# Kernel optimization log

Hardware: AMD Instinct MI355X
Metric: run time of the kernel (lower is better)

Reference implementation:

```python
import jax, jax.numpy as jnp
import numpy as np

B, NPTS, H, O, L, PDIM, CDIM = 16, 20000, 128, 4, 6, 8, 3
K = 3  # number of learnable sine terms in Rowdy activation


def setup_inputs() -> dict:
    key = jax.random.key(0)
    ks = jax.random.split(key, 12)
    sc = lambda fan: 1.0 / np.sqrt(fan)
    return {
        "coords": jax.random.normal(ks[0], (B, NPTS, CDIM), dtype=jnp.float32),
        "sdf": jax.random.normal(ks[1], (B, NPTS, 1), dtype=jnp.float32),
        "params": jax.random.normal(ks[2], (B, PDIM), dtype=jnp.float32),
        # branch MLP: PDIM -> H (xL hidden) -> H*O
        "branch_W0": jax.random.normal(ks[3], (PDIM, H)) * sc(PDIM),
        "branch_Wr": jax.random.normal(ks[4], (L - 1, H, H)) * sc(H),
        "branch_b": jnp.zeros((L, H)),
        "branch_Wout": jax.random.normal(ks[5], (H, H * O)) * sc(H),
        "branch_bout": jnp.zeros((H * O,)),
        # trunk MLP: (CDIM+1) -> H (xL) with Rowdy activations
        "trunk_W0": jax.random.normal(ks[6], (CDIM + 1, H)) * sc(CDIM + 1),
        "trunk_Wr": jax.random.normal(ks[7], (L - 1, H, H)) * sc(H),
        "trunk_b": jnp.zeros((L, H)),
        "rowdy_a": 0.1 * jax.random.normal(ks[8], (L, K, H)),
        "final_W": jax.random.normal(ks[9], (H, H)) * sc(H),
        "final_b": jnp.zeros((H,)),
    }


def _rowdy(z, a):
    # Rowdy activation: tanh(z) + sum_k a_k * sin(k*z); a: (K, H)
    out = jnp.tanh(z)
    for k in range(a.shape[0]):
        out = out + a[k] * jnp.sin((k + 1.0) * z)
    return out


def reference(coords, sdf, params, branch_W0, branch_Wr, branch_b,
              branch_Wout, branch_bout, trunk_W0, trunk_Wr, trunk_b,
              rowdy_a, final_W, final_b):
    # ---- branch tower (records post-activation hiddens) ----
    h = jnp.tanh(params @ branch_W0 + branch_b[0])        # (B, H)
    hiddens = [h]
    for i in range(1, L):
        h = jnp.tanh(h @ branch_Wr[i - 1] + branch_b[i])
        hiddens.append(h)
    branch_out = h @ branch_Wout + branch_bout             # (B, H*O)
    # cumulative skip sums S_i = sum_{j<=i} hidden_j
    S = [hiddens[0]]
    for i in range(1, L):
        S.append(hiddens[i] + S[-1])
    # ---- trunk tower with fusion by accumulated branch features ----
    x = jnp.concatenate([coords, sdf], axis=-1)            # (B, NPTS, CDIM+1)
    for i in range(L):
        W = trunk_W0 if i == 0 else trunk_Wr[i - 1]
        x = _rowdy(x @ W + trunk_b[i], rowdy_a[i])         # (B, NPTS, H)
        x = x * S[i][:, None, :]                           # broadcast multiply
    YL = x @ final_W + final_b                             # (B, NPTS, H)
    ZL = branch_out.reshape(B, O, H)
    # sum(ZL * YL, -1) as batched contraction over H
    return jnp.einsum('boh,bnh->bno', ZL, YL)              # (B, NPTS, O)
```

## Files before the change

kernel.cpp:

```cpp
#include <hip/hip_runtime.h>
#include <hip/hip_bf16.h>
#include <stdint.h>

#define B_    16
#define NPTS_ 20000
#define H_    128
#define O_    4
#define L_    6
#define PDIM_ 8
#define K_    3

#define TPTS 64
#define KSTR 136
#define TILES_PER_B ((NPTS_ + TPTS - 1) / TPTS)

typedef __attribute__((ext_vector_type(8))) short short8;
typedef __attribute__((ext_vector_type(4))) float f32x4;
typedef __attribute__((ext_vector_type(4))) unsigned short us4;

__device__ __forceinline__ uint16_t f2bf(float x) {
    uint32_t u = __float_as_uint(x);
    uint32_t r = u + 0x7FFFu + ((u >> 16) & 1u);
    return (uint16_t)(r >> 16);
}
__device__ __forceinline__ float bf2f(uint16_t h) {
    return __uint_as_float(((uint32_t)h) << 16);
}

__device__ __forceinline__ float rowdy_act(float z, float a0, float a1, float a2) {
    float e  = __expf(2.f * z);
    float th = 1.f - 2.f * __builtin_amdgcn_rcpf(e + 1.f);
    float s1 = __sinf(z);
    float c1 = __cosf(z);
    float s2 = 2.f * s1 * c1;
    float s3 = s1 * (3.f - 4.f * s1 * s1);
    return th + a0 * s1 + a1 * s2 + a2 * s3;
}
__device__ __forceinline__ void act_split(float z, float a0, float a1, float a2,
                                          float s, uint16_t& h, uint16_t& l) {
    float x = rowdy_act(z, a0, a1, a2) * s;
    h = f2bf(x);
    l = f2bf(x - bf2f(h));
}

__global__ void prep_w(const float* __restrict__ tWr,
                       uint16_t* __restrict__ WtHi, uint16_t* __restrict__ WtLo) {
    const int bid = blockIdx.x;
    const int l   = bid >> 7;
    const int j   = bid & 127;
    const int k   = threadIdx.x;
    float w = tWr[((size_t)l * H_ + k) * H_ + j];
    uint16_t h = f2bf(w);
    uint16_t lo = f2bf(w - bf2f(h));
    WtHi[((size_t)l * H_ + j) * H_ + k] = h;
    WtLo[((size_t)l * H_ + j) * H_ + k] = lo;
}

__global__ void branch_kernel(
    const float* __restrict__ params,
    const float* __restrict__ bW0, const float* __restrict__ bWr,
    const float* __restrict__ bb,  const float* __restrict__ bWout,
    const float* __restrict__ bbout,
    const float* __restrict__ fW,  const float* __restrict__ fb,
    float* __restrict__ S, float* __restrict__ M, float* __restrict__ c0)
{
    const int b = blockIdx.x;
    const int j = threadIdx.x;
    __shared__ float h[H_];
    __shared__ float zl[O_][H_];

    float z = bb[j];
    #pragma unroll
    for (int k = 0; k < PDIM_; ++k)
        z = fmaf(params[b * PDIM_ + k], bW0[k * H_ + j], z);
    float hv = tanhf(z);
    float srun = hv;
    h[j] = hv;
    S[(0 * B_ + b) * H_ + j] = srun;

    for (int i = 1; i < L_; ++i) {
        __syncthreads();
        const float* W = bWr + (size_t)(i - 1) * H_ * H_;
        float zz = bb[i * H_ + j];
        for (int k = 0; k < H_; ++k)
            zz = fmaf(h[k], W[k * H_ + j], zz);
        __syncthreads();
        hv = tanhf(zz);
        h[j] = hv;
        srun += hv;
        S[(i * B_ + b) * H_ + j] = srun;
    }
    __syncthreads();

    #pragma unroll
    for (int o = 0; o < O_; ++o) {
        float acc = bbout[o * H_ + j];
        for (int k = 0; k < H_; ++k)
            acc = fmaf(h[k], bWout[(size_t)k * (H_ * O_) + o * H_ + j], acc);
        zl[o][j] = acc;
    }
    __syncthreads();

    float m[O_] = {0.f, 0.f, 0.f, 0.f};
    for (int hh = 0; hh < H_; ++hh) {
        float w = fW[j * H_ + hh];
        #pragma unroll
        for (int o = 0; o < O_; ++o)
            m[o] = fmaf(w, zl[o][hh], m[o]);
    }
    #pragma unroll
    for (int o = 0; o < O_; ++o)
        M[((size_t)b * H_ + j) * O_ + o] = m[o];

    if (j < O_) {
        float acc = 0.f;
        for (int hh = 0; hh < H_; ++hh)
            acc = fmaf(fb[hh], zl[j][hh], acc);
        c0[b * O_ + j] = acc;
    }
}

__global__ __launch_bounds__(256, 4) void trunk_mfma(
    const float* __restrict__ coords, const float* __restrict__ sdf,
    const float* __restrict__ tW0,    const float* __restrict__ tb,
    const float* __restrict__ ra,     const float* __restrict__ S,
    const float* __restrict__ M,      const float* __restrict__ c0,
    const uint16_t* __restrict__ WtHi, const uint16_t* __restrict__ WtLo,
    float* __restrict__ out)
{
    __shared__ __align__(16) uint16_t Xhi[TPTS][KSTR];
    __shared__ __align__(16) uint16_t Xlo[TPTS][KSTR];

    const int blk  = blockIdx.x;
    const int b    = blk / TILES_PER_B;
    const int tile = blk % TILES_PER_B;
    const int p0   = tile * TPTS;
    const int t    = threadIdx.x;

    {
        const int p = t >> 2;
        const int q = t & 3;
        int pg = p0 + p;
        int pc = pg < NPTS_ ? pg : NPTS_ - 1;
        size_t gp = (size_t)b * NPTS_ + pc;
        float in0 = coords[gp * 3 + 0], in1 = coords[gp * 3 + 1];
        float in2 = coords[gp * 3 + 2], in3 = sdf[gp];
        #pragma unroll
        for (int jj = 0; jj < 32; jj += 4) {
            const int j = q * 32 + jj;
            float4 w0 = *(const float4*)(tW0 + 0 * H_ + j);
            float4 w1 = *(const float4*)(tW0 + 1 * H_ + j);
            float4 w2 = *(const float4*)(tW0 + 2 * H_ + j);
            float4 w3 = *(const float4*)(tW0 + 3 * H_ + j);
            float4 bv = *(const float4*)(tb + j);
            float4 A0 = *(const float4*)(ra + 0 * H_ + j);
            float4 A1 = *(const float4*)(ra + 1 * H_ + j);
            float4 A2 = *(const float4*)(ra + 2 * H_ + j);
            float4 Sv = *(const float4*)(S + b * H_ + j);
            float z0 = fmaf(in3, w3.x, fmaf(in2, w2.x, fmaf(in1, w1.x, fmaf(in0, w0.x, bv.x))));
            float z1 = fmaf(in3, w3.y, fmaf(in2, w2.y, fmaf(in1, w1.y, fmaf(in0, w0.y, bv.y))));
            float z2 = fmaf(in3, w3.z, fmaf(in2, w2.z, fmaf(in1, w1.z, fmaf(in0, w0.z, bv.z))));
            float z3 = fmaf(in3, w3.w, fmaf(in2, w2.w, fmaf(in1, w1.w, fmaf(in0, w0.w, bv.w))));
            us4 h4, l4;
            uint16_t hh, ll;
            act_split(z0, A0.x, A1.x, A2.x, Sv.x, hh, ll); h4[0] = hh; l4[0] = ll;
            act_split(z1, A0.y, A1.y, A2.y, Sv.y, hh, ll); h4[1] = hh; l4[1] = ll;
            act_split(z2, A0.z, A1.z, A2.z, Sv.z, hh, ll); h4[2] = hh; l4[2] = ll;
            act_split(z3, A0.w, A1.w, A2.w, Sv.w, hh, ll); h4[3] = hh; l4[3] = ll;
            *(us4*)(&Xhi[p][j]) = h4;
            *(us4*)(&Xlo[p][j]) = l4;
        }
    }
    __syncthreads();

    const int ln    = t & 63;
    const int wv    = t >> 6;
    const int l15   = ln & 15;
    const int l4    = ln >> 4;
    const int jbase = wv * 32;

    for (int layer = 1; layer < L_; ++layer) {
        f32x4 acc[2][4];
        #pragma unroll
        for (int jf = 0; jf < 2; ++jf) {
            const int j = jbase + jf * 16 + l4 * 4;
            float4 bv = *(const float4*)(tb + layer * H_ + j);
            #pragma unroll
            for (int pf = 0; pf < 4; ++pf)
                acc[jf][pf] = (f32x4){bv.x, bv.y, bv.z, bv.w};
        }
        const uint16_t* WH = WtHi + (size_t)(layer - 1) * H_ * H_;
        const uint16_t* WL = WtLo + (size_t)(layer - 1) * H_ * H_;
        #pragma unroll
        for (int ks = 0; ks < 4; ++ks) {
            const int kpos = ks * 32 + l4 * 8;
            short8 aH[2], aL[2];
            #pragma unroll
            for (int jf = 0; jf < 2; ++jf) {
                const int j = jbase + jf * 16 + l15;
                aH[jf] = *(const short8*)(WH + (size_t)j * H_ + kpos);
                aL[jf] = *(const short8*)(WL + (size_t)j * H_ + kpos);
            }
            #pragma unroll
            for (int pf = 0; pf < 4; ++pf) {
                const int prow = pf * 16 + l15;
                short8 bH = *(const short8*)(&Xhi[prow][kpos]);
                short8 bL = *(const short8*)(&Xlo[prow][kpos]);
                #pragma unroll
                for (int jf = 0; jf < 2; ++jf) {
                    acc[jf][pf] = __builtin_amdgcn_mfma_f32_16x16x32_bf16(aH[jf], bH, acc[jf][pf], 0, 0, 0);
                    acc[jf][pf] = __builtin_amdgcn_mfma_f32_16x16x32_bf16(aH[jf], bL, acc[jf][pf], 0, 0, 0);
                    acc[jf][pf] = __builtin_amdgcn_mfma_f32_16x16x32_bf16(aL[jf], bH, acc[jf][pf], 0, 0, 0);
                }
            }
        }
        __syncthreads();

        #pragma unroll
        for (int jf = 0; jf < 2; ++jf) {
            const int j = jbase + jf * 16 + l4 * 4;
            float4 A0 = *(const float4*)(ra + (layer * K_ + 0) * H_ + j);
            float4 A1 = *(const float4*)(ra + (layer * K_ + 1) * H_ + j);
            float4 A2 = *(const float4*)(ra + (layer * K_ + 2) * H_ + j);
            float4 Sv = *(const float4*)(S + (layer * B_ + b) * H_ + j);
            #pragma unroll
            for (int pf = 0; pf < 4; ++pf) {
                const int prow = pf * 16 + l15;
                us4 h4, l4v;
                uint16_t hh, ll;
                act_split(acc[jf][pf][0], A0.x, A1.x, A2.x, Sv.x, hh, ll); h4[0] = hh; l4v[0] = ll;
                act_split(acc[jf][pf][1], A0.y, A1.y, A2.y, Sv.y, hh, ll); h4[1] = hh; l4v[1] = ll;
                act_split(acc[jf][pf][2], A0.z, A1.z, A2.z, Sv.z, hh, ll); h4[2] = hh; l4v[2] = ll;
                act_split(acc[jf][pf][3], A0.w, A1.w, A2.w, Sv.w, hh, ll); h4[3] = hh; l4v[3] = ll;
                *(us4*)(&Xhi[prow][j]) = h4;
                *(us4*)(&Xlo[prow][j]) = l4v;
            }
        }
        __syncthreads();
    }

    {
        const int p = t >> 2;
        const int o = t & 3;
        float acc = c0[b * O_ + o];
        const float* Mb = M + (size_t)b * H_ * O_;
        #pragma unroll 4
        for (int k = 0; k < H_; k += 8) {
            short8 h8 = *(const short8*)(&Xhi[p][k]);
            short8 l8 = *(const short8*)(&Xlo[p][k]);
            #pragma unroll
            for (int e = 0; e < 8; ++e) {
                float xv = bf2f((uint16_t)h8[e]) + bf2f((uint16_t)l8[e]);
                acc = fmaf(xv, Mb[(k + e) * O_ + o], acc);
            }
        }
        int gp = p0 + p;
        if (gp < NPTS_)
            out[((size_t)b * NPTS_ + gp) * O_ + o] = acc;
    }
}

extern "C" void kernel_launch(void* const* d_in, const int* in_sizes, int n_in,
                              void* d_out, int out_size, void* d_ws, size_t ws_size,
                              hipStream_t stream) {
    const float* coords  = (const float*)d_in[0];
    const float* sdf     = (const float*)d_in[1];
    const float* params  = (const float*)d_in[2];
    const float* bW0     = (const float*)d_in[3];
    const float* bWr     = (const float*)d_in[4];
    const float* bb      = (const float*)d_in[5];
    const float* bWout   = (const float*)d_in[6];
    const float* bbout   = (const float*)d_in[7];
    const float* tW0     = (const float*)d_in[8];
    const float* tWr     = (const float*)d_in[9];
    const float* tb      = (const float*)d_in[10];
    const float* ra      = (const float*)d_in[11];
    const float* fW      = (const float*)d_in[12];
    const float* fb      = (const float*)d_in[13];
    float* out = (float*)d_out;

    float* S  = (float*)d_ws;
    float* M  = S + (size_t)L_ * B_ * H_;
    float* c0 = M + (size_t)B_ * H_ * O_;
    uint16_t* WtHi = (uint16_t*)(c0 + B_ * O_);
    uint16_t* WtLo = WtHi + (size_t)(L_ - 1) * H_ * H_;

    prep_w<<<dim3((L_ - 1) * H_), dim3(H_), 0, stream>>>(tWr, WtHi, WtLo);
    branch_kernel<<<dim3(B_), dim3(H_), 0, stream>>>(
        params, bW0, bWr, bb, bWout, bbout, fW, fb, S, M, c0);
    trunk_mfma<<<dim3(B_ * TILES_PER_B), dim3(256), 0, stream>>>(
        coords, sdf, tW0, tb, ra, S, M, c0, WtHi, WtLo, out);
}
```

Baseline: 522.4 us.

## Store weights and activations in MFMA fragment order and pack bf16 via hardware cvt

Lays out the hi/lo bf16 weight copies in global memory and the activation tile in shared memory in MFMA fragment order. Each lane now does contiguous 16-byte loads with no padded strides. Activation packing uses v_cvt_pk_bf16_f32 instead of manual rounding. The hi weight fragments for all k-steps are also preloaded into registers before the MFMA loop. This is meant to cut LDS bank conflicts, address arithmetic and conversion ALU work, at the cost of more register pressure and a more complex index mapping.

```diff
diff --git a/kernel.cpp b/kernel.cpp
--- a/kernel.cpp
+++ b/kernel.cpp
@@ -11,20 +11,27 @@
 #define K_    3
 
 #define TPTS 64
-#define KSTR 136
 #define TILES_PER_B ((NPTS_ + TPTS - 1) / TPTS)
 
 typedef __attribute__((ext_vector_type(8))) short short8;
 typedef __attribute__((ext_vector_type(4))) float f32x4;
-typedef __attribute__((ext_vector_type(4))) unsigned short us4;
-
+typedef __attribute__((ext_vector_type(2))) uint32_t u32x2;
+typedef __attribute__((ext_vector_type(4))) uint32_t u32x4;
+
+#define FRAG(ks, pf, pl, lane) ((((((ks)*4 + (pf))*2 + (pl))*64) + (lane))*8)
+
+__device__ __forceinline__ uint32_t cvt_pk_bf16(float a, float b) {
+    uint32_t d;
+    asm("v_cvt_pk_bf16_f32 %0, %1, %2" : "=v"(d) : "v"(a), "v"(b));
+    return d;
+}
+__device__ __forceinline__ float bf2f(uint16_t h) {
+    return __uint_as_float(((uint32_t)h) << 16);
+}
 __device__ __forceinline__ uint16_t f2bf(float x) {
     uint32_t u = __float_as_uint(x);
     uint32_t r = u + 0x7FFFu + ((u >> 16) & 1u);
     return (uint16_t)(r >> 16);
-}
-__device__ __forceinline__ float bf2f(uint16_t h) {
-    return __uint_as_float(((uint32_t)h) << 16);
 }
 
 __device__ __forceinline__ float rowdy_act(float z, float a0, float a1, float a2) {
@@ -36,24 +43,47 @@
     float s3 = s1 * (3.f - 4.f * s1 * s1);
     return th + a0 * s1 + a1 * s2 + a2 * s3;
 }
-__device__ __forceinline__ void act_split(float z, float a0, float a1, float a2,
-                                          float s, uint16_t& h, uint16_t& l) {
-    float x = rowdy_act(z, a0, a1, a2) * s;
-    h = f2bf(x);
-    l = f2bf(x - bf2f(h));
+
+__device__ __forceinline__ void act_pack4(const f32x4& v,
+                                          const float4& A0, const float4& A1,
+                                          const float4& A2, const float4& Sv,
+                                          u32x2& hi, u32x2& lo) {
+    float x0 = rowdy_act(v[0], A0.x, A1.x, A2.x) * Sv.x;
+    float x1 = rowdy_act(v[1], A0.y, A1.y, A2.y) * Sv.y;
+    float x2 = rowdy_act(v[2], A0.z, A1.z, A2.z) * Sv.z;
+    float x3 = rowdy_act(v[3], A0.w, A1.w, A2.w) * Sv.w;
+    uint32_t d0 = cvt_pk_bf16(x0, x1);
+    uint32_t d1 = cvt_pk_bf16(x2, x3);
+    float r0 = x0 - __uint_as_float(d0 << 16);
+    float r1 = x1 - __uint_as_float(d0 & 0xFFFF0000u);
+    float r2 = x2 - __uint_as_float(d1 << 16);
+    float r3 = x3 - __uint_as_float(d1 & 0xFFFF0000u);
+    hi = (u32x2){d0, d1};
+    lo = (u32x2){cvt_pk_bf16(r0, r1), cvt_pk_bf16(r2, r3)};
 }
 
 __global__ void prep_w(const float* __restrict__ tWr,
-                       uint16_t* __restrict__ WtHi, uint16_t* __restrict__ WtLo) {
-    const int bid = blockIdx.x;
-    const int l   = bid >> 7;
-    const int j   = bid & 127;
-    const int k   = threadIdx.x;
-    float w = tWr[((size_t)l * H_ + k) * H_ + j];
-    uint16_t h = f2bf(w);
-    uint16_t lo = f2bf(w - bf2f(h));
-    WtHi[((size_t)l * H_ + j) * H_ + k] = h;
-    WtLo[((size_t)l * H_ + j) * H_ + k] = lo;
+                       uint16_t* __restrict__ WfH, uint16_t* __restrict__ WfL) {
+    const int bid   = blockIdx.x;
+    const int layer = bid >> 3;
+    const int wv    = (bid >> 1) & 3;
+    const int jf    = bid & 1;
+    const int t     = threadIdx.x;
+    const int ks    = t >> 6;
+    const int ln    = t & 63;
+    const int j     = wv * 32 + jf * 16 + (ln & 15);
+    const int kbase = ks * 32 + (ln >> 4) * 8;
+    uint16_t hi[8], lo[8];
+    #pragma unroll
+    for (int e = 0; e < 8; ++e) {
+        float w = tWr[((size_t)layer * H_ + kbase + e) * H_ + j];
+        uint16_t h = f2bf(w);
+        hi[e] = h;
+        lo[e] = f2bf(w - bf2f(h));
+    }
+    size_t dst = ((size_t)((((layer * 4 + wv) * 2 + jf) * 4 + ks) * 64 + ln)) * 8;
+    #pragma unroll
+    for (int e = 0; e < 8; ++e) { WfH[dst + e] = hi[e]; WfL[dst + e] = lo[e]; }
 }
 
 __global__ void branch_kernel(
@@ -125,11 +155,10 @@
     const float* __restrict__ tW0,    const float* __restrict__ tb,
     const float* __restrict__ ra,     const float* __restrict__ S,
     const float* __restrict__ M,      const float* __restrict__ c0,
-    const uint16_t* __restrict__ WtHi, const uint16_t* __restrict__ WtLo,
+    const uint16_t* __restrict__ WfH, const uint16_t* __restrict__ WfL,
     float* __restrict__ out)
 {
-    __shared__ __align__(16) uint16_t Xhi[TPTS][KSTR];
-    __shared__ __align__(16) uint16_t Xlo[TPTS][KSTR];
+    __shared__ __align__(16) uint16_t Xf[4 * 4 * 2 * 64 * 8];
 
     const int blk  = blockIdx.x;
     const int b    = blk / TILES_PER_B;
@@ -138,37 +167,42 @@
     const int t    = threadIdx.x;
 
     {
-        const int p = t >> 2;
-        const int q = t & 3;
+        const int p   = t >> 2;
+        const int q   = t & 3;
+        const int pf  = p >> 4;
+        const int p15 = p & 15;
         int pg = p0 + p;
         int pc = pg < NPTS_ ? pg : NPTS_ - 1;
         size_t gp = (size_t)b * NPTS_ + pc;
         float in0 = coords[gp * 3 + 0], in1 = coords[gp * 3 + 1];
         float in2 = coords[gp * 3 + 2], in3 = sdf[gp];
         #pragma unroll
-        for (int jj = 0; jj < 32; jj += 4) {
-            const int j = q * 32 + jj;
-            float4 w0 = *(const float4*)(tW0 + 0 * H_ + j);
-            float4 w1 = *(const float4*)(tW0 + 1 * H_ + j);
-            float4 w2 = *(const float4*)(tW0 + 2 * H_ + j);
-            float4 w3 = *(const float4*)(tW0 + 3 * H_ + j);
-            float4 bv = *(const float4*)(tb + j);
-            float4 A0 = *(const float4*)(ra + 0 * H_ + j);
-            float4 A1 = *(const float4*)(ra + 1 * H_ + j);
-            float4 A2 = *(const float4*)(ra + 2 * H_ + j);
-            float4 Sv = *(const float4*)(S + b * H_ + j);
-            float z0 = fmaf(in3, w3.x, fmaf(in2, w2.x, fmaf(in1, w1.x, fmaf(in0, w0.x, bv.x))));
-            float z1 = fmaf(in3, w3.y, fmaf(in2, w2.y, fmaf(in1, w1.y, fmaf(in0, w0.y, bv.y))));
-            float z2 = fmaf(in3, w3.z, fmaf(in2, w2.z, fmaf(in1, w1.z, fmaf(in0, w0.z, bv.z))));
-            float z3 = fmaf(in3, w3.w, fmaf(in2, w2.w, fmaf(in1, w1.w, fmaf(in0, w0.w, bv.w))));
-            us4 h4, l4;
-            uint16_t hh, ll;
-            act_split(z0, A0.x, A1.x, A2.x, Sv.x, hh, ll); h4[0] = hh; l4[0] = ll;
-            act_split(z1, A0.y, A1.y, A2.y, Sv.y, hh, ll); h4[1] = hh; l4[1] = ll;
-            act_split(z2, A0.z, A1.z, A2.z, Sv.z, hh, ll); h4[2] = hh; l4[2] = ll;
-            act_split(z3, A0.w, A1.w, A2.w, Sv.w, hh, ll); h4[3] = hh; l4[3] = ll;
-            *(us4*)(&Xhi[p][j]) = h4;
-            *(us4*)(&Xlo[p][j]) = l4;
+        for (int m = 0; m < 4; ++m) {
+            const int jo = q * 32 + m * 8;
+            u32x2 hiA, loA, hiB, loB;
+            #pragma unroll
+            for (int half = 0; half < 2; ++half) {
+                const int j = jo + half * 4;
+                float4 w0 = *(const float4*)(tW0 + 0 * H_ + j);
+                float4 w1 = *(const float4*)(tW0 + 1 * H_ + j);
+                float4 w2 = *(const float4*)(tW0 + 2 * H_ + j);
+                float4 w3 = *(const float4*)(tW0 + 3 * H_ + j);
+                float4 bv = *(const float4*)(tb + j);
+                float4 A0 = *(const float4*)(ra + 0 * H_ + j);
+                float4 A1 = *(const float4*)(ra + 1 * H_ + j);
+                float4 A2 = *(const float4*)(ra + 2 * H_ + j);
+                float4 Sv = *(const float4*)(S + b * H_ + j);
+                f32x4 zv;
+                zv[0] = fmaf(in3, w3.x, fmaf(in2, w2.x, fmaf(in1, w1.x, fmaf(in0, w0.x, bv.x))));
+                zv[1] = fmaf(in3, w3.y, fmaf(in2, w2.y, fmaf(in1, w1.y, fmaf(in0, w0.y, bv.y))));
+                zv[2] = fmaf(in3, w3.z, fmaf(in2, w2.z, fmaf(in1, w1.z, fmaf(in0, w0.z, bv.z))));
+                zv[3] = fmaf(in3, w3.w, fmaf(in2, w2.w, fmaf(in1, w1.w, fmaf(in0, w0.w, bv.w))));
+                if (half == 0) act_pack4(zv, A0, A1, A2, Sv, hiA, loA);
+                else           act_pack4(zv, A0, A1, A2, Sv, hiB, loB);
+            }
+            const int lane = m * 16 + p15;
+            *(u32x4*)(&Xf[FRAG(q, pf, 0, lane)]) = (u32x4){hiA[0], hiA[1], hiB[0], hiB[1]};
+            *(u32x4*)(&Xf[FRAG(q, pf, 1, lane)]) = (u32x4){loA[0], loA[1], loB[0], loB[1]};
         }
     }
     __syncthreads();
@@ -189,33 +223,35 @@
             for (int pf = 0; pf < 4; ++pf)
                 acc[jf][pf] = (f32x4){bv.x, bv.y, bv.z, bv.w};
         }
-        const uint16_t* WH = WtHi + (size_t)(layer - 1) * H_ * H_;
-        const uint16_t* WL = WtLo + (size_t)(layer - 1) * H_ * H_;
+        const uint16_t* WHb = WfH + ((size_t)((layer - 1) * 4 + wv) * 2) * 4 * 64 * 8;
+        const uint16_t* WLb = WfL + ((size_t)((layer - 1) * 4 + wv) * 2) * 4 * 64 * 8;
+        short8 aH[2][4];
+        #pragma unroll
+        for (int jf = 0; jf < 2; ++jf)
+            #pragma unroll
+            for (int ks = 0; ks < 4; ++ks)
+                aH[jf][ks] = *(const short8*)(WHb + ((size_t)(jf * 4 + ks) * 64 + ln) * 8);
+
         #pragma unroll
         for (int ks = 0; ks < 4; ++ks) {
-            const int kpos = ks * 32 + l4 * 8;
-            short8 aH[2], aL[2];
-            #pragma unroll
-            for (int jf = 0; jf < 2; ++jf) {
-                const int j = jbase + jf * 16 + l15;
-                aH[jf] = *(const short8*)(WH + (size_t)j * H_ + kpos);
-                aL[jf] = *(const short8*)(WL + (size_t)j * H_ + kpos);
+            short8 aL0 = *(const short8*)(WLb + ((size_t)(0 * 4 + ks) * 64 + ln) * 8);
+            short8 aL1 = *(const short8*)(WLb + ((size_t)(1 * 4 + ks) * 64 + ln) * 8);
+            #pragma unroll
+            for (int pf = 0; pf < 4; ++pf) {
+                short8 bH = *(const short8*)(&Xf[FRAG(ks, pf, 0, ln)]);
+                short8 bL = *(const short8*)(&Xf[FRAG(ks, pf, 1, ln)]);
+                acc[0][pf] = __builtin_amdgcn_mfma_f32_16x16x32_bf16(aH[0][ks], bH, acc[0][pf], 0, 0, 0);
+                acc[0][pf] = __builtin_amdgcn_mfma_f32_16x16x32_bf16(aH[0][ks], bL, acc[0][pf], 0, 0, 0);
+                acc[0][pf] = __builtin_amdgcn_mfma_f32_16x16x32_bf16(aL0,       bH, acc[0][pf], 0, 0, 0);
+                acc[1][pf] = __builtin_amdgcn_mfma_f32_16x16x32_bf16(aH[1][ks], bH, acc[1][pf], 0, 0, 0);
+                acc[1][pf] = __builtin_amdgcn_mfma_f32_16x16x32_bf16(aH[1][ks], bL, acc[1][pf], 0, 0, 0);
+                acc[1][pf] = __builtin_amdgcn_mfma_f32_16x16x32_bf16(aL1,       bH, acc[1][pf], 0, 0, 0);
             }
-            #pragma unroll
-            for (int pf = 0; pf < 4; ++pf) {
-                const int prow = pf * 16 + l15;
-                short8 bH = *(const short8*)(&Xhi[prow][kpos]);
-                short8 bL = *(const short8*)(&Xlo[prow][kpos]);
-                #pragma unroll
-                for (int jf = 0; jf < 2; ++jf) {
-                    acc[jf][pf] = __builtin_amdgcn_mfma_f32_16x16x32_bf16(aH[jf], bH, acc[jf][pf], 0, 0, 0);
-                    acc[jf][pf] = __builtin_amdgcn_mfma_f32_16x16x32_bf16(aH[jf], bL, acc[jf][pf], 0, 0, 0);
-                    acc[jf][pf] = __builtin_amdgcn_mfma_f32_16x16x32_bf16(aL[jf], bH, acc[jf][pf], 0, 0, 0);
-                }
-            }
         }
         __syncthreads();
 
+        const int l4p  = l4 >> 1;
+        const int eoff = (l4 & 1) * 4;
         #pragma unroll
         for (int jf = 0; jf < 2; ++jf) {
             const int j = jbase + jf * 16 + l4 * 4;
@@ -223,35 +259,38 @@
             float4 A1 = *(const float4*)(ra + (layer * K_ + 1) * H_ + j);
             float4 A2 = *(const float4*)(ra + (layer * K_ + 2) * H_ + j);
             float4 Sv = *(const float4*)(S + (layer * B_ + b) * H_ + j);
+            const int lanep = (jf * 2 + l4p) * 16 + l15;
             #pragma unroll
             for (int pf = 0; pf < 4; ++pf) {
-                const int prow = pf * 16 + l15;
-                us4 h4, l4v;
-                uint16_t hh, ll;
-                act_split(acc[jf][pf][0], A0.x, A1.x, A2.x, Sv.x, hh, ll); h4[0] = hh; l4v[0] = ll;
-                act_split(acc[jf][pf][1], A0.y, A1.y, A2.y, Sv.y, hh, ll); h4[1] = hh; l4v[1] = ll;
-                act_split(acc[jf][pf][2], A0.z, A1.z, A2.z, Sv.z, hh, ll); h4[2] = hh; l4v[2] = ll;
-                act_split(acc[jf][pf][3], A0.w, A1.w, A2.w, Sv.w, hh, ll); h4[3] = hh; l4v[3] = ll;
-                *(us4*)(&Xhi[prow][j]) = h4;
-                *(us4*)(&Xlo[prow][j]) = l4v;
+                u32x2 hi, lo;
+                act_pack4(acc[jf][pf], A0, A1, A2, Sv, hi, lo);
+                *(u32x2*)(&Xf[FRAG(wv, pf, 0, lanep) + eoff]) = hi;
+                *(u32x2*)(&Xf[FRAG(wv, pf, 1, lanep) + eoff]) = lo;
             }
         }
         __syncthreads();
     }
 
     {
-        const int p = t >> 2;
-        const int o = t & 3;
+        const int p   = t >> 2;
+        const int o   = t & 3;
+        const int pf  = p >> 4;
+        const int p15 = p & 15;
         float acc = c0[b * O_ + o];
         const float* Mb = M + (size_t)b * H_ * O_;
-        #pragma unroll 4
-        for (int k = 0; k < H_; k += 8) {
-            short8 h8 = *(const short8*)(&Xhi[p][k]);
-            short8 l8 = *(const short8*)(&Xlo[p][k]);
-            #pragma unroll
-            for (int e = 0; e < 8; ++e) {
-                float xv = bf2f((uint16_t)h8[e]) + bf2f((uint16_t)l8[e]);
-                acc = fmaf(xv, Mb[(k + e) * O_ + o], acc);
+        #pragma unroll
+        for (int ks = 0; ks < 4; ++ks) {
+            #pragma unroll
+            for (int m = 0; m < 4; ++m) {
+                const int lane = m * 16 + p15;
+                short8 h8 = *(const short8*)(&Xf[FRAG(ks, pf, 0, lane)]);
+                short8 l8 = *(const short8*)(&Xf[FRAG(ks, pf, 1, lane)]);
+                const int kb = ks * 32 + m * 8;
+                #pragma unroll
+                for (int e = 0; e < 8; ++e) {
+                    float xv = bf2f((uint16_t)h8[e]) + bf2f((uint16_t)l8[e]);
+                    acc = fmaf(xv, Mb[(kb + e) * O_ + o], acc);
+                }
             }
         }
         int gp = p0 + p;
@@ -282,12 +321,12 @@
     float* S  = (float*)d_ws;
     float* M  = S + (size_t)L_ * B_ * H_;
     float* c0 = M + (size_t)B_ * H_ * O_;
-    uint16_t* WtHi = (uint16_t*)(c0 + B_ * O_);
-    uint16_t* WtLo = WtHi + (size_t)(L_ - 1) * H_ * H_;
-
-    prep_w<<<dim3((L_ - 1) * H_), dim3(H_), 0, stream>>>(tWr, WtHi, WtLo);
+    uint16_t* WfH = (uint16_t*)(c0 + B_ * O_);
+    uint16_t* WfL = WfH + (size_t)(L_ - 1) * H_ * H_;
+
+    prep_w<<<dim3((L_ - 1) * 4 * 2), dim3(256), 0, stream>>>(tWr, WfH, WfL);
     branch_kernel<<<dim3(B_), dim3(H_), 0, stream>>>(
         params, bW0, bWr, bb, bWout, bbout, fW, fb, S, M, c0);
     trunk_mfma<<<dim3(B_ * TILES_PER_B), dim3(256), 0, stream>>>(
-        coords, sdf, tW0, tb, ra, S, M, c0, WtHi, WtLo, out);
-}
+        coords, sdf, tW0, tb, ra, S, M, c0, WfH, WfL, out);
+}
```

After: 665.9 us. 27.4% more time.
